# Optimization experiments

Measured on AMD Instinct MI355X. Metric: run time of the kernel, lower is better.

## Reference

```python
import jax, jax.numpy as jnp
import numpy as np

D_MODEL = 1024
M = 64            # oscillators; state dim N = 2*M
N = 2 * M
N_H = 2           # Householder reflections per step
DT = 0.1
OMEGA_MAX = 100.0
BATCH, SEQ = 8, 2048


def setup_inputs() -> dict:
    key = jax.random.key(0)
    ks = jax.random.split(key, 8)
    u = jax.random.normal(ks[0], (BATCH, SEQ, D_MODEL), jnp.float32)
    # learned parameters (scaled like the module's small-gain init)
    W_A = jax.random.normal(ks[1], (M, D_MODEL), jnp.float32) * 0.01
    b_A = jnp.zeros((M,), jnp.float32)
    W_k = jax.random.normal(ks[2], (N_H, N, D_MODEL), jnp.float32) * 0.02
    b_k = jnp.zeros((N_H, N), jnp.float32)
    W_beta = jax.random.normal(ks[3], (N_H, D_MODEL), jnp.float32) * 0.02
    b_beta = jnp.zeros((N_H,), jnp.float32)
    B_w = jax.random.normal(ks[4], (N, D_MODEL), jnp.float32) * 0.02
    B_b = jnp.zeros((N,), jnp.float32)
    C = jax.random.normal(ks[5], (D_MODEL, N), jnp.float32) * 0.01
    D = jax.random.normal(ks[6], (D_MODEL,), jnp.float32) * 0.01
    return dict(u=u, W_A=W_A, b_A=b_A, W_k=W_k, b_k=b_k,
                W_beta=W_beta, b_beta=b_beta, B_w=B_w, B_b=B_b, C=C, D=D)


def reference(u, W_A, b_A, W_k, b_k, W_beta, b_beta, B_w, B_b, C, D):
    batch = u.shape[0]
    # --- precompute all input-dependent per-step quantities as big GEMMs ---
    A = jax.nn.relu(jnp.einsum('btd,md->btm', u, W_A) + b_A)
    A = jnp.minimum(A, OMEGA_MAX)                       # clamp(max=omega_max)
    S = 1.0 / (1.0 + (DT * DT) * A)                     # (B,T,M)
    K = jnp.einsum('btd,jnd->btjn', u, W_k) + b_k       # (B,T,n_h,N)
    K = K / jnp.maximum(jnp.linalg.norm(K, axis=-1, keepdims=True), 1e-12)
    beta = 2.0 * jax.nn.sigmoid(jnp.einsum('btd,jd->btj', u, W_beta) + b_beta)
    Bt = jnp.einsum('btd,nd->btn', u, B_w) + B_b        # (B,T,N)

    # time-major for scan
    xs = (jnp.moveaxis(A, 1, 0), jnp.moveaxis(S, 1, 0), jnp.moveaxis(K, 1, 0),
          jnp.moveaxis(beta, 1, 0), jnp.moveaxis(Bt, 1, 0))
    h0 = jnp.zeros((batch, N), u.dtype)

    def step(h, x):
        A_t, S_t, K_t, beta_t, B_t = x
        # oscillatory rotation-contraction R_t @ h (m 2x2 blocks)
        z, y = h[:, :M], h[:, M:]
        z_new = S_t * z - DT * A_t * S_t * y
        y_new = DT * S_t * z + S_t * y
        h = jnp.concatenate([z_new, y_new], axis=-1)
        # sequential Householder product H_t @ h (fixed small n_h loop)
        for j in range(N_H):
            k = K_t[:, j]                                # (B,N), unit norm
            dot = jnp.sum(k * h, axis=-1, keepdims=True)
            h = h - beta_t[:, j:j + 1] * k * dot
        h = h + B_t
        return h, h

    _, hs = jax.lax.scan(step, h0, xs)                  # (T,B,N)
    hs = jnp.moveaxis(hs, 0, 1)                         # (B,T,N)
    return jnp.einsum('btn,dn->btd', hs, C) + u * D
```

## Files before the change

kernel.cpp:

```cpp
#include <hip/hip_runtime.h>
#include <cmath>


#define NTOK 16384
#define TT 2048
#define BB 8
#define DM 1024
#define FS 520
#define CH 64
#define LCH 32
#define NCH 512
#define NW 448
#define NWP 512

typedef short bf16x8 __attribute__((ext_vector_type(8)));
typedef float f32x4 __attribute__((ext_vector_type(4)));

#define GLOAD_LDS16(g, l)                                          \
  __builtin_amdgcn_global_load_lds(                                \
      (const __attribute__((address_space(1))) void*)(g),          \
      (__attribute__((address_space(3))) void*)(l), 16, 0, 0)

#define RAW_BAR() do {                                             \
    asm volatile("s_waitcnt lgkmcnt(0)" ::: "memory");             \
    __builtin_amdgcn_sched_barrier(0);                             \
    __builtin_amdgcn_s_barrier();                                  \
    __builtin_amdgcn_sched_barrier(0);                             \
  } while (0)

#define WAIT_VM(N) do {                                            \
    __builtin_amdgcn_sched_barrier(0);                             \
    asm volatile("s_waitcnt vmcnt(" #N ")" ::: "memory");          \
    __builtin_amdgcn_sched_barrier(0);                             \
  } while (0)

__global__ __launch_bounds__(256) void packW(
    const float* __restrict__ W_A, const float* __restrict__ b_A,
    const float* __restrict__ W_k, const float* __restrict__ b_k,
    const float* __restrict__ b_beta,
    const float* __restrict__ B_w, const float* __restrict__ B_b,
    float* __restrict__ Wp, float* __restrict__ bias) {
  int r = blockIdx.x;
  int tid = threadIdx.x;
  const float* src;
  float bv;
  if (r < 64)       { src = W_A + (size_t)r * DM;         bv = b_A[r]; }
  else if (r < 320) { src = W_k + (size_t)(r - 64) * DM;  bv = b_k[r - 64]; }
  else              { src = B_w + (size_t)(r - 320) * DM; bv = B_b[r - 320]; }
  ((float4*)(Wp + (size_t)r * DM))[tid] = ((const float4*)src)[tid];
  if (tid == 0) bias[r] = bv;
  if (r == 0 && tid < 2) bias[448 + tid] = b_beta[tid];
}

__device__ inline unsigned short bf16_rne(float x) {
  unsigned b = __float_as_uint(x);
  b += 0x7FFFu + ((b >> 16) & 1u);
  return (unsigned short)(b >> 16);
}

__device__ inline void split_bf16(float x, unsigned short& h, unsigned short& l) {
  unsigned b = __float_as_uint(x);
  h = (unsigned short)(b >> 16);
  float rem = x - __uint_as_float(b & 0xFFFF0000u);
  l = bf16_rne(rem);
}

__global__ __launch_bounds__(256) void convertU(
    const float* __restrict__ u, unsigned short* __restrict__ uh,
    unsigned short* __restrict__ ul) {
  int gid = blockIdx.x * 256 + threadIdx.x;
  int m = gid >> 8;
  int g = gid & 255;
  float4 v = *(const float4*)(u + (size_t)m * DM + g * 4);
  int kt = g >> 3, gg = g & 7;
  int p = gg & 3, h = gg >> 2;
  int mr = m & 127, mb = m >> 7;
  int pp = p ^ ((mr >> 2) & 3);
  size_t dst = ((size_t)(mb * 32 + kt)) * 4096 + mr * 32 + ((pp << 1) | h) * 4;
  ushort4 hi, lo;
  split_bf16(v.x, hi.x, lo.x);
  split_bf16(v.y, hi.y, lo.y);
  split_bf16(v.z, hi.z, lo.z);
  split_bf16(v.w, hi.w, lo.w);
  *(ushort4*)(uh + dst) = hi;
  *(ushort4*)(ul + dst) = lo;
}

__global__ __launch_bounds__(256) void convertW(
    const float* __restrict__ Wp, unsigned short* __restrict__ Wb) {
  int gid = blockIdx.x * 256 + threadIdx.x;
  int n = gid >> 8, g = gid & 255;
  int kt = g >> 3, gg = g & 7;
  int p = gg & 3, h = gg >> 2;
  int nr = n & 127, nb = n >> 7;
  int pp = p ^ ((nr >> 2) & 3);
  size_t dst = ((size_t)(nb * 32 + kt)) * 4096 + nr * 32 + ((pp << 1) | h) * 4;
  ushort4 hv = make_ushort4(0, 0, 0, 0);
  if (n < NW) {
    float4 v = *(const float4*)(Wp + (size_t)n * DM + g * 4);
    hv.x = bf16_rne(v.x); hv.y = bf16_rne(v.y);
    hv.z = bf16_rne(v.z); hv.w = bf16_rne(v.w);
  }
  *(ushort4*)(Wb + dst) = hv;
}

__global__ __launch_bounds__(256) void convertC(
    const float* __restrict__ Cm, unsigned short* __restrict__ Chp,
    unsigned short* __restrict__ Clp) {
  int gid = blockIdx.x * 256 + threadIdx.x;
  int d = gid >> 5;
  int g = gid & 31;
  float4 v = *(const float4*)(Cm + (size_t)d * 128 + g * 4);
  int kt = g >> 3, gg = g & 7;
  int p = gg & 3, h = gg >> 2;
  int nr = d & 127, nb = d >> 7;
  int pp = p ^ ((nr >> 2) & 3);
  size_t dst = ((size_t)(nb * 4 + kt)) * 4096 + nr * 32 + ((pp << 1) | h) * 4;
  ushort4 hi, lo;
  split_bf16(v.x, hi.x, lo.x);
  split_bf16(v.y, hi.y, lo.y);
  split_bf16(v.z, hi.z, lo.z);
  split_bf16(v.w, hi.w, lo.w);
  *(ushort4*)(Chp + dst) = hi;
  *(ushort4*)(Clp + dst) = lo;
}

__global__ __launch_bounds__(256) void gemmA_mfma(
    const unsigned short* __restrict__ uh, const unsigned short* __restrict__ ul,
    const unsigned short* __restrict__ Wb, float* __restrict__ Feat) {
  __shared__ __align__(16) unsigned short As[8192];
  __shared__ __align__(16) unsigned short Bs[8192];
  const int tid = threadIdx.x;
  const int wv = tid >> 6, ln = tid & 63;
  const int lr = ln & 15, G = ln >> 4;
  const int wm = wv >> 1, wn = wv & 1;
  const int x = G ^ (lr >> 2);
  f32x4 acc[4][4];
#pragma unroll
  for (int i = 0; i < 4; ++i)
#pragma unroll
    for (int j = 0; j < 4; ++j) acc[i][j] = (f32x4){0.f, 0.f, 0.f, 0.f};

  const size_t aBase = (size_t)blockIdx.x * 32 * 4096;
  const size_t bBase = (size_t)blockIdx.y * 32 * 4096;
  const int so = wv * 512 + ln * 8;
  const int ld = wv * 512;

  auto stage = [&](int step, int buf) {
    const unsigned short* pa = (step < 32) ? uh : ul;
    const int kt = step & 31;
    const unsigned short* ga = pa + aBase + (size_t)kt * 4096;
    const unsigned short* gb = Wb + bBase + (size_t)kt * 4096;
    unsigned short* A = As + buf * 4096;
    unsigned short* B = Bs + buf * 4096;
    GLOAD_LDS16(ga + so,        A + ld);
    GLOAD_LDS16(ga + 2048 + so, A + 2048 + ld);
    GLOAD_LDS16(gb + so,        B + ld);
    GLOAD_LDS16(gb + 2048 + so, B + 2048 + ld);
  };

  stage(0, 0);
  __syncthreads();
  for (int s = 0; s < 64; ++s) {
    const int cur = s & 1;
    if (s + 1 < 64) stage(s + 1, cur ^ 1);
    bf16x8 af[4], bfr[4];
    const char* Ab = (const char*)(As + cur * 4096) + ((wm * 64 + lr) << 6) + (x << 4);
    const char* Bb = (const char*)(Bs + cur * 4096) + ((wn * 64 + lr) << 6) + (x << 4);
#pragma unroll
    for (int i = 0; i < 4; ++i) {
      af[i]  = *(const bf16x8*)(Ab + i * 1024);
      bfr[i] = *(const bf16x8*)(Bb + i * 1024);
    }
#pragma unroll
    for (int i = 0; i < 4; ++i)
#pragma unroll
      for (int j = 0; j < 4; ++j)
        acc[i][j] = __builtin_amdgcn_mfma_f32_16x16x32_bf16(
            af[i], bfr[j], acc[i][j], 0, 0, 0);
    __syncthreads();
  }
  const int row0 = (blockIdx.x << 7) + wm * 64 + (G << 2);
  const int col0 = (blockIdx.y << 7) + wn * 64 + lr;
  float* fb = Feat + (size_t)row0 * FS + col0;
#pragma unroll
  for (int i = 0; i < 4; ++i)
#pragma unroll
    for (int j = 0; j < 4; ++j) {
      float* d = fb + (size_t)(i * 16) * FS + j * 16;
#pragma unroll
      for (int r = 0; r < 4; ++r) d[(size_t)r * FS] = acc[i][j][r];
    }
}

__global__ __launch_bounds__(256) void gemmC_mfma(
    const unsigned short* __restrict__ hsh, const unsigned short* __restrict__ hsl,
    const unsigned short* __restrict__ Chp, const unsigned short* __restrict__ Clp,
    const float* __restrict__ u, const float* __restrict__ Dv,
    float* __restrict__ out) {
  __shared__ __align__(16) unsigned short As[8192];
  __shared__ __align__(16) unsigned short Bs[8192];
  const int tid = threadIdx.x;
  const int wv = tid >> 6, ln = tid & 63;
  const int lr = ln & 15, G = ln >> 4;
  const int wm = wv >> 1, wn = wv & 1;
  const int x = G ^ (lr >> 2);
  f32x4 acc[4][4];
#pragma unroll
  for (int i = 0; i < 4; ++i)
#pragma unroll
    for (int j = 0; j < 4; ++j) acc[i][j] = (f32x4){0.f, 0.f, 0.f, 0.f};

  const size_t aBase = (size_t)blockIdx.x * 4 * 4096;
  const size_t bBase = (size_t)blockIdx.y * 4 * 4096;
  const int so = wv * 512 + ln * 8;
  const int ld = wv * 512;

  auto stage = [&](int step, int buf) {
    const int pass = step >> 2, kt = step & 3;
    const unsigned short* pa = (pass == 1) ? hsl : hsh;
    const unsigned short* pb = (pass == 2) ? Clp : Chp;
    const unsigned short* ga = pa + aBase + (size_t)kt * 4096;
    const unsigned short* gb = pb + bBase + (size_t)kt * 4096;
    unsigned short* A = As + buf * 4096;
    unsigned short* B = Bs + buf * 4096;
    GLOAD_LDS16(ga + so,        A + ld);
    GLOAD_LDS16(ga + 2048 + so, A + 2048 + ld);
    GLOAD_LDS16(gb + so,        B + ld);
    GLOAD_LDS16(gb + 2048 + so, B + 2048 + ld);
  };

  stage(0, 0);
  __syncthreads();
  for (int s = 0; s < 12; ++s) {
    const int cur = s & 1;
    if (s + 1 < 12) stage(s + 1, cur ^ 1);
    bf16x8 af[4], bfr[4];
    const char* Ab = (const char*)(As + cur * 4096) + ((wm * 64 + lr) << 6) + (x << 4);
    const char* Bb = (const char*)(Bs + cur * 4096) + ((wn * 64 + lr) << 6) + (x << 4);
#pragma unroll
    for (int i = 0; i < 4; ++i) {
      af[i]  = *(const bf16x8*)(Ab + i * 1024);
      bfr[i] = *(const bf16x8*)(Bb + i * 1024);
    }
#pragma unroll
    for (int i = 0; i < 4; ++i)
#pragma unroll
      for (int j = 0; j < 4; ++j)
        acc[i][j] = __builtin_amdgcn_mfma_f32_16x16x32_bf16(
            af[i], bfr[j], acc[i][j], 0, 0, 0);
    __syncthreads();
  }
  const int row0 = (blockIdx.x << 7) + wm * 64 + (G << 2);
  const int col0 = (blockIdx.y << 7) + wn * 64 + lr;
#pragma unroll
  for (int j = 0; j < 4; ++j) {
    float dv = Dv[col0 + j * 16];
#pragma unroll
    for (int i = 0; i < 4; ++i) {
#pragma unroll
      for (int r = 0; r < 4; ++r) {
        size_t off = (size_t)(row0 + i * 16 + r) * DM + col0 + j * 16;
        out[off] = fmaf(u[off], dv, acc[i][j][r]);
      }
    }
  }
}

__device__ inline float wave_sum(float v) {
#pragma unroll
  for (int off = 32; off > 0; off >>= 1) v += __shfl_xor(v, off, 64);
  return v;
}

__global__ __launch_bounds__(64) void postA(float* __restrict__ Feat,
                                            const float* __restrict__ bias,
                                            const float* __restrict__ u,
                                            const float* __restrict__ Wb) {
  const int t = blockIdx.x, lane = threadIdx.x;
  float* f = Feat + (size_t)t * FS;
  float s0 = 0.f, s1 = 0.f;
#pragma unroll
  for (int j = 0; j < 4; ++j) {
    float4 uv = *(const float4*)(u + (size_t)t * DM + j * 256 + lane * 4);
    float4 w0 = *(const float4*)(Wb + j * 256 + lane * 4);
    float4 w1 = *(const float4*)(Wb + DM + j * 256 + lane * 4);
    s0 = fmaf(uv.x, w0.x, s0); s0 = fmaf(uv.y, w0.y, s0);
    s0 = fmaf(uv.z, w0.z, s0); s0 = fmaf(uv.w, w0.w, s0);
    s1 = fmaf(uv.x, w1.x, s1); s1 = fmaf(uv.y, w1.y, s1);
    s1 = fmaf(uv.z, w1.z, s1); s1 = fmaf(uv.w, w1.w, s1);
  }
  s0 = wave_sum(s0); s1 = wave_sum(s1);
  float a = f[lane] + bias[lane];
  a = fminf(fmaxf(a, 0.f), 100.f);
  float S = 1.f / (1.f + 0.01f * a);
  f[lane] = S;
  f[448 + lane] = 0.1f * a * S;
  float k10 = f[64 + lane] + bias[64 + lane];
  float k11 = f[128 + lane] + bias[128 + lane];
  float n1 = wave_sum(k10 * k10 + k11 * k11);
  float inv1 = 1.f / fmaxf(sqrtf(n1), 1e-12f);
  k10 *= inv1; k11 *= inv1;
  f[64 + lane] = k10; f[128 + lane] = k11;
  float k20 = f[192 + lane] + bias[192 + lane];
  float k21 = f[256 + lane] + bias[256 + lane];
  float n2 = wave_sum(k20 * k20 + k21 * k21);
  float inv2 = 1.f / fmaxf(sqrtf(n2), 1e-12f);
  k20 *= inv2; k21 *= inv2;
  f[192 + lane] = k20; f[256 + lane] = k21;
  float c12 = wave_sum(k10 * k20 + k11 * k21);
  if (lane == 0) {
    f[512] = 2.f / (1.f + expf(-(s0 + bias[448])));
    f[513] = 2.f / (1.f + expf(-(s1 + bias[449])));
    f[514] = c12;
  }
  f[320 + lane] += bias[320 + lane];
  f[384 + lane] += bias[384 + lane];
}

__global__ __launch_bounds__(512, 2) void scanB1(
    const float* __restrict__ Feat, float* __restrict__ Mc) {
  const int cid = blockIdx.x;
  const int t0 = (cid >> 6) * TT + (cid & 63) * LCH;
  const int tid = threadIdx.x;
  const int col = tid >> 2, q = tid & 3;
  const int i0 = q * 16;
  __shared__ float fb[2][4 * FS];
  float mz[16], my[16];
#pragma unroll
  for (int j = 0; j < 16; ++j) {
    mz[j] = (i0 + j == col) ? 1.f : 0.f;
    my[j] = (64 + i0 + j == col) ? 1.f : 0.f;
  }
  {
    const float4* src = (const float4*)(Feat + (size_t)t0 * FS);
    for (int v = tid; v < FS; v += 512) ((float4*)fb[0])[v] = src[v];
  }
  __syncthreads();
  for (int g = 0; g < LCH / 4; ++g) {
    const int cur = g & 1;
    float4 pf0, pf1;
    const bool has2 = tid < (FS - 512);
    if (g < LCH / 4 - 1) {
      const float4* src = (const float4*)(Feat + (size_t)(t0 + (g + 1) * 4) * FS);
      pf0 = src[tid];
      if (has2) pf1 = src[tid + 512];
    }
#pragma unroll
    for (int s = 0; s < 4; ++s) {
      const float* f = fb[cur] + s * FS;
      float sj[16], cj[16], k1z[16], k1y[16], k2z[16], k2y[16];
#pragma unroll
      for (int v = 0; v < 4; ++v) {
        *(float4*)&sj[4 * v]  = *(const float4*)(f + i0 + 4 * v);
        *(float4*)&cj[4 * v]  = *(const float4*)(f + 448 + i0 + 4 * v);
        *(float4*)&k1z[4 * v] = *(const float4*)(f + 64 + i0 + 4 * v);
        *(float4*)&k1y[4 * v] = *(const float4*)(f + 128 + i0 + 4 * v);
        *(float4*)&k2z[4 * v] = *(const float4*)(f + 192 + i0 + 4 * v);
        *(float4*)&k2y[4 * v] = *(const float4*)(f + 256 + i0 + 4 * v);
      }
      float4 sc = *(const float4*)(f + 512);
      float p = 0.f, r2 = 0.f;
#pragma unroll
      for (int j = 0; j < 16; ++j) {
        float s0 = sj[j], c1 = cj[j];
        float z = mz[j], y = my[j];
        float sz = s0 * z;
        z = fmaf(-c1, y, sz);
        y = fmaf(s0, y, 0.1f * sz);
        mz[j] = z; my[j] = y;
        p  = fmaf(k1z[j], z, p);  p  = fmaf(k1y[j], y, p);
        r2 = fmaf(k2z[j], z, r2); r2 = fmaf(k2y[j], y, r2);
      }
      p  += __shfl_xor(p, 1, 64);  p  += __shfl_xor(p, 2, 64);
      r2 += __shfl_xor(r2, 1, 64); r2 += __shfl_xor(r2, 2, 64);
      float e1 = sc.x * p;
      float e2 = sc.y * fmaf(-sc.z, e1, r2);
#pragma unroll
      for (int j = 0; j < 16; ++j) {
        float z = fmaf(-e1, k1z[j], mz[j]);
        mz[j] = fmaf(-e2, k2z[j], z);
        float y = fmaf(-e1, k1y[j], my[j]);
        my[j] = fmaf(-e2, k2y[j], y);
      }
    }
    if (g < LCH / 4 - 1) {
      ((float4*)fb[1 - cur])[tid] = pf0;
      if (has2) ((float4*)fb[1 - cur])[tid + 512] = pf1;
    }
    __syncthreads();
  }
  float* dst = Mc + ((size_t)cid * 128 + col) * 128;
#pragma unroll
  for (int v = 0; v < 4; ++v)
    *(float4*)(dst + i0 + 4 * v) = *(float4*)&mz[4 * v];
#pragma unroll
  for (int v = 0; v < 4; ++v)
    *(float4*)(dst + 64 + i0 + 4 * v) = *(float4*)&my[4 * v];
}

__global__ __launch_bounds__(64) void scanB0(
    const float* __restrict__ Feat, float* __restrict__ dc) {
  const int cid = blockIdx.x;
  const int lane = threadIdx.x;
  float z = 0.f, y = 0.f;
  const int t0 = (cid >> 6) * TT + (cid & 63) * LCH;
  for (int t = t0; t < t0 + LCH; ++t) {
    const float* __restrict__ f = Feat + (size_t)t * FS;
    float s = f[lane], c1 = f[448 + lane];
    float k1z = f[64 + lane], k1y = f[128 + lane];
    float k2z = f[192 + lane], k2y = f[256 + lane];
    float bz = f[320 + lane], by = f[384 + lane];
    float b1 = f[512], b2 = f[513], c12 = f[514];
    float sz = s * z;
    float zn = fmaf(-c1, y, sz);
    float yn = fmaf(s, y, 0.1f * sz);
    float p = fmaf(k1y, yn, k1z * zn);
    float qq = fmaf(k2y, yn, k2z * zn);
#pragma unroll
    for (int off = 32; off > 0; off >>= 1) {
      p += __shfl_xor(p, off, 64);
      qq += __shfl_xor(qq, off, 64);
    }
    float e1 = b1 * p;
    float d2 = fmaf(-c12, e1, qq);
    float e2 = b2 * d2;
    z = fmaf(-e1, k1z, zn); z = fmaf(-e2, k2z, z); z += bz;
    y = fmaf(-e1, k1y, yn); y = fmaf(-e2, k2y, y); y += by;
  }
  dc[(size_t)cid * 128 + lane] = z;
  dc[(size_t)cid * 128 + 64 + lane] = y;
}

__global__ __launch_bounds__(1024, 1) void scanB2(
    const float* __restrict__ Mc, const float* __restrict__ dc,
    float* __restrict__ hstart) {
  const int b = blockIdx.x;
  const int tid = threadIdx.x;
  const int i = tid & 127, jh = tid >> 7;
  const int wv = tid >> 6;
  __shared__ __align__(16) float Ms[2][16384];
  __shared__ float h[128];
  __shared__ float red[8][128];
  if (tid < 128) h[tid] = 0.f;

  auto stage = [&](int cn, int buf) {
    const float* g = Mc + (size_t)(b * CH + cn) * 16384;
#pragma unroll
    for (int q = 0; q < 4; ++q) {
      const float* gp = g + q * 4096 + wv * 256 + (tid & 63) * 4;
      float* lp = Ms[buf] + q * 4096 + wv * 256;
      GLOAD_LDS16(gp, lp);
    }
  };

  stage(0, 0);
  float d0 = dc[(size_t)(b * CH) * 128 + i];
  __syncthreads();

  int cur = 0;
  for (int c = 0; c < CH; ++c) {
    const int cn = (c + 1) & (CH - 1);
    stage(cn, cur ^ 1);
    float d1 = dc[(size_t)(b * CH + cn) * 128 + i];
    WAIT_VM(5);
    RAW_BAR();
    if (tid < 128) hstart[(size_t)(b * CH + c) * 128 + tid] = h[tid];
    float acc = 0.f;
#pragma unroll
    for (int j = 0; j < 16; ++j)
      acc = fmaf(Ms[cur][(jh * 16 + j) * 128 + i], h[jh * 16 + j], acc);
    red[jh][i] = acc;
    RAW_BAR();
    if (tid < 128) {
      float sum = d0;
#pragma unroll
      for (int k = 0; k < 8; ++k) sum += red[k][tid];
      h[tid] = sum;
    }
    d0 = d1;
    cur ^= 1;
  }
}

__global__ __launch_bounds__(64) void scanB3(
    const float* __restrict__ Feat, const float* __restrict__ hstart,
    unsigned short* __restrict__ hsh, unsigned short* __restrict__ hsl) {
  const int cid = blockIdx.x;
  const int lane = threadIdx.x;
  float z = hstart[(size_t)cid * 128 + lane];
  float y = hstart[(size_t)cid * 128 + 64 + lane];
  const int t0 = (cid >> 6) * TT + (cid & 63) * LCH;
  const int ktz = lane >> 5, kkz = lane & 31;
  const int kty = (64 + lane) >> 5;
  const int pz = (kkz >> 2) & 3, hz = kkz >> 4;
  const int lowz = kkz & 3;
  for (int t = t0; t < t0 + LCH; ++t) {
    const float* __restrict__ f = Feat + (size_t)t * FS;
    float s = f[lane], c1 = f[448 + lane];
    float k1z = f[64 + lane], k1y = f[128 + lane];
    float k2z = f[192 + lane], k2y = f[256 + lane];
    float bz = f[320 + lane], by = f[384 + lane];
    float b1 = f[512], b2 = f[513], c12 = f[514];
    float sz = s * z;
    float zn = fmaf(-c1, y, sz);
    float yn = fmaf(s, y, 0.1f * sz);
    float p = fmaf(k1y, yn, k1z * zn);
    float qq = fmaf(k2y, yn, k2z * zn);
#pragma unroll
    for (int off = 32; off > 0; off >>= 1) {
      p += __shfl_xor(p, off, 64);
      qq += __shfl_xor(qq, off, 64);
    }
    float e1 = b1 * p;
    float d2 = fmaf(-c12, e1, qq);
    float e2 = b2 * d2;
    zn = fmaf(-e1, k1z, zn); zn = fmaf(-e2, k2z, zn); zn += bz;
    yn = fmaf(-e1, k1y, yn); yn = fmaf(-e2, k2y, yn); yn += by;
    {
      const int mb = t >> 7, mr = t & 127;
      const int xr = (mr >> 2) & 3;
      size_t idxz = ((size_t)(mb * 4 + ktz)) * 4096 + mr * 32 +
                    ((((pz ^ xr) << 1) | hz)) * 4 + lowz;
      size_t idxy = ((size_t)(mb * 4 + kty)) * 4096 + mr * 32 +
                    ((((pz ^ xr) << 1) | hz)) * 4 + lowz;
      unsigned short hi, lo;
      split_bf16(zn, hi, lo);
      hsh[idxz] = hi; hsl[idxz] = lo;
      split_bf16(yn, hi, lo);
      hsh[idxy] = hi; hsl[idxy] = lo;
    }
    z = zn; y = yn;
  }
}

extern "C" void kernel_launch(void* const* d_in, const int* in_sizes, int n_in,
                              void* d_out, int out_size, void* d_ws, size_t ws_size,
                              hipStream_t stream) {
  const float* u      = (const float*)d_in[0];
  const float* W_A    = (const float*)d_in[1];
  const float* b_A    = (const float*)d_in[2];
  const float* W_k    = (const float*)d_in[3];
  const float* b_k    = (const float*)d_in[4];
  const float* W_beta = (const float*)d_in[5];
  const float* b_beta = (const float*)d_in[6];
  const float* B_w    = (const float*)d_in[7];
  const float* B_b    = (const float*)d_in[8];
  const float* Cm     = (const float*)d_in[9];
  const float* Dv     = (const float*)d_in[10];
  float* out = (float*)d_out;
  char* ws = (char*)d_ws;
  float* Wp     = (float*)(ws);
  unsigned short* Wb = (unsigned short*)(ws + 1835008);
  float* bias   = (float*)(ws + 4194304);
  float* Feat   = (float*)(ws + 4198400);
  unsigned short* uh = (unsigned short*)(ws + 38277120);
  float* Mc     = (float*)(ws + 38277120);
  unsigned short* ul = (unsigned short*)(ws + 71831552);
  unsigned short* hsh = (unsigned short*)(ws + 71831552);
  unsigned short* hsl = (unsigned short*)(ws + 76025856);
  unsigned short* Chp = (unsigned short*)(ws + 80220160);
  unsigned short* Clp = (unsigned short*)(ws + 80482304);
  float* dcv    = (float*)(ws + 80744448);
  float* hstart = (float*)(ws + 81006592);

  packW<<<dim3(448), dim3(256), 0, stream>>>(W_A, b_A, W_k, b_k, b_beta,
                                             B_w, B_b, Wp, bias);
  convertW<<<dim3(512), dim3(256), 0, stream>>>(Wp, Wb);
  convertU<<<dim3(16384), dim3(256), 0, stream>>>(u, uh, ul);
  gemmA_mfma<<<dim3(128, 4), dim3(256), 0, stream>>>(uh, ul, Wb, Feat);
  convertC<<<dim3(128), dim3(256), 0, stream>>>(Cm, Chp, Clp);
  postA<<<dim3(16384), dim3(64), 0, stream>>>(Feat, bias, u, W_beta);
  scanB1<<<dim3(NCH), dim3(512), 0, stream>>>(Feat, Mc);
  scanB0<<<dim3(NCH), dim3(64), 0, stream>>>(Feat, dcv);
  scanB2<<<dim3(8), dim3(1024), 0, stream>>>(Mc, dcv, hstart);
  scanB3<<<dim3(NCH), dim3(64), 0, stream>>>(Feat, hstart, hsh, hsl);
  gemmC_mfma<<<dim3(128, 8), dim3(256), 0, stream>>>(hsh, hsl, Chp, Clp,
                                                     u, Dv, out);
}
```

Measured before the change: 423.9 us.

## Split chunk-carry scan across four blocks per batch with global flag sync

The sequential chunk-carry propagation was one 1024-thread block per batch, streaming each 128x128 chunk matrix through LDS. It is now four 256-thread blocks per batch, each owning 32 output rows, which hold their matrix slice in registers and exchange the full state through global memory using per-chunk atomic counters with acquire/release spinning. The aim is to spread the serial chain across more CUs and cut per-step LDS staging and reduction. The cost is a cross-block global round-trip and spin-wait every chunk. It also relies on all 32 blocks being co-resident, and the spin loop has a timeout guard.

Result: slower. 500.0 us (+18.0%).

```diff
diff --git a/kernel.cpp b/kernel.cpp
--- a/kernel.cpp
+++ b/kernel.cpp
@@ -20,19 +20,6 @@
   __builtin_amdgcn_global_load_lds(                                \
       (const __attribute__((address_space(1))) void*)(g),          \
       (__attribute__((address_space(3))) void*)(l), 16, 0, 0)
-
-#define RAW_BAR() do {                                             \
-    asm volatile("s_waitcnt lgkmcnt(0)" ::: "memory");             \
-    __builtin_amdgcn_sched_barrier(0);                             \
-    __builtin_amdgcn_s_barrier();                                  \
-    __builtin_amdgcn_sched_barrier(0);                             \
-  } while (0)
-
-#define WAIT_VM(N) do {                                            \
-    __builtin_amdgcn_sched_barrier(0);                             \
-    asm volatile("s_waitcnt vmcnt(" #N ")" ::: "memory");          \
-    __builtin_amdgcn_sched_barrier(0);                             \
-  } while (0)
 
 __global__ __launch_bounds__(256) void packW(
     const float* __restrict__ W_A, const float* __restrict__ b_A,
@@ -400,9 +387,13 @@
 }
 
 __global__ __launch_bounds__(64) void scanB0(
-    const float* __restrict__ Feat, float* __restrict__ dc) {
+    const float* __restrict__ Feat, float* __restrict__ dc,
+    int* __restrict__ flags) {
   const int cid = blockIdx.x;
   const int lane = threadIdx.x;
+  if (cid == 0) {
+    for (int i = lane; i < 512; i += 64) flags[i] = 0;
+  }
   float z = 0.f, y = 0.f;
   const int t0 = (cid >> 6) * TT + (cid & 63) * LCH;
   for (int t = t0; t < t0 + LCH; ++t) {
@@ -432,54 +423,61 @@
   dc[(size_t)cid * 128 + 64 + lane] = y;
 }
 
-__global__ __launch_bounds__(1024, 1) void scanB2(
+__global__ __launch_bounds__(256) void scanB2x(
     const float* __restrict__ Mc, const float* __restrict__ dc,
-    float* __restrict__ hstart) {
-  const int b = blockIdx.x;
+    float* __restrict__ hstart, int* __restrict__ flags) {
+  const int bid = blockIdx.x;
+  const int b = bid >> 2, g = bid & 3;
   const int tid = threadIdx.x;
-  const int i = tid & 127, jh = tid >> 7;
-  const int wv = tid >> 6;
-  __shared__ __align__(16) float Ms[2][16384];
-  __shared__ float h[128];
-  __shared__ float red[8][128];
-  if (tid < 128) h[tid] = 0.f;
-
-  auto stage = [&](int cn, int buf) {
-    const float* g = Mc + (size_t)(b * CH + cn) * 16384;
-#pragma unroll
-    for (int q = 0; q < 4; ++q) {
-      const float* gp = g + q * 4096 + wv * 256 + (tid & 63) * 4;
-      float* lp = Ms[buf] + q * 4096 + wv * 256;
-      GLOAD_LDS16(gp, lp);
-    }
-  };
-
-  stage(0, 0);
-  float d0 = dc[(size_t)(b * CH) * 128 + i];
+  const int s = tid >> 5, r = tid & 31;
+  const int R = g * 32 + r;
+  __shared__ float dl[CH][32];
+  __shared__ float red[8][32];
+  __shared__ float hcur[128];
+  for (int idx = tid; idx < CH * 32; idx += 256) {
+    int c = idx >> 5, rr = idx & 31;
+    dl[c][rr] = dc[(size_t)(b * CH + c) * 128 + g * 32 + rr];
+  }
+  if (tid < 32) hstart[(size_t)(b * CH) * 128 + g * 32 + tid] = 0.f;
+  if (tid < 128) hcur[tid] = 0.f;
   __syncthreads();
 
-  int cur = 0;
   for (int c = 0; c < CH; ++c) {
-    const int cn = (c + 1) & (CH - 1);
-    stage(cn, cur ^ 1);
-    float d1 = dc[(size_t)(b * CH + cn) * 128 + i];
-    WAIT_VM(5);
-    RAW_BAR();
-    if (tid < 128) hstart[(size_t)(b * CH + c) * 128 + tid] = h[tid];
+    const float* Mp = Mc + ((size_t)(b * CH + c) * 128 + s * 16) * 128 + R;
+    float m[16];
+#pragma unroll
+    for (int j = 0; j < 16; ++j) m[j] = Mp[(size_t)j * 128];
+    if (c > 0) {
+      if (tid == 0) {
+        int guard = 0;
+        while (__hip_atomic_load(&flags[b * 64 + c], __ATOMIC_ACQUIRE,
+                                 __HIP_MEMORY_SCOPE_AGENT) < 4) {
+          __builtin_amdgcn_s_sleep(1);
+          if (++guard > (1 << 26)) break;
+        }
+      }
+      __syncthreads();
+      if (tid < 128) hcur[tid] = hstart[(size_t)(b * CH + c) * 128 + tid];
+      __syncthreads();
+    }
     float acc = 0.f;
 #pragma unroll
-    for (int j = 0; j < 16; ++j)
-      acc = fmaf(Ms[cur][(jh * 16 + j) * 128 + i], h[jh * 16 + j], acc);
-    red[jh][i] = acc;
-    RAW_BAR();
-    if (tid < 128) {
-      float sum = d0;
-#pragma unroll
-      for (int k = 0; k < 8; ++k) sum += red[k][tid];
-      h[tid] = sum;
-    }
-    d0 = d1;
-    cur ^= 1;
+    for (int j = 0; j < 16; ++j) acc = fmaf(m[j], hcur[s * 16 + j], acc);
+    red[s][r] = acc;
+    __syncthreads();
+    if (c + 1 < CH) {
+      if (tid < 32) {
+        float sum = dl[c][tid];
+#pragma unroll
+        for (int k = 0; k < 8; ++k) sum += red[k][tid];
+        hstart[(size_t)(b * CH + c + 1) * 128 + g * 32 + tid] = sum;
+        __threadfence();
+      }
+      __syncthreads();
+      if (tid == 0)
+        __hip_atomic_fetch_add(&flags[b * 64 + c + 1], 1, __ATOMIC_RELEASE,
+                               __HIP_MEMORY_SCOPE_AGENT);
+    }
   }
 }
 
@@ -563,6 +561,7 @@
   unsigned short* Clp = (unsigned short*)(ws + 80482304);
   float* dcv    = (float*)(ws + 80744448);
   float* hstart = (float*)(ws + 81006592);
+  int* flags    = (int*)(ws + 81268736);
 
   packW<<<dim3(448), dim3(256), 0, stream>>>(W_A, b_A, W_k, b_k, b_beta,
                                              B_w, B_b, Wp, bias);
@@ -572,8 +571,8 @@
   convertC<<<dim3(128), dim3(256), 0, stream>>>(Cm, Chp, Clp);
   postA<<<dim3(16384), dim3(64), 0, stream>>>(Feat, bias, u, W_beta);
   scanB1<<<dim3(NCH), dim3(512), 0, stream>>>(Feat, Mc);
-  scanB0<<<dim3(NCH), dim3(64), 0, stream>>>(Feat, dcv);
-  scanB2<<<dim3(8), dim3(1024), 0, stream>>>(Mc, dcv, hstart);
+  scanB0<<<dim3(NCH), dim3(64), 0, stream>>>(Feat, dcv, flags);
+  scanB2x<<<dim3(32), dim3(256), 0, stream>>>(Mc, dcv, hstart, flags);
   scanB3<<<dim3(NCH), dim3(64), 0, stream>>>(Feat, hstart, hsh, hsl);
   gemmC_mfma<<<dim3(128, 8), dim3(256), 0, stream>>>(hsh, hsl, Chp, Clp,
                                                      u, Dv, out);
```

## Fuse weight packing into convertW and register-prefetch Mc in scanB2

Applied to the files above, without the earlier changes.

Removes the packW kernel by having convertW read W_A/W_k/B_w directly and write the bias vector from one block, saving a launch and an intermediate fp32 copy. In scanB2, the double-buffered LDS staging of the 64KB chunk transition matrix via global_load_lds is replaced by per-thread register prefetch of 16 matrix entries for the next chunk. This trades LDS occupancy and async copies for register loads and adds an extra barrier per chunk.

New measurement: 401.6 us. 1.06x faster.

```diff
diff --git a/kernel.cpp b/kernel.cpp
--- a/kernel.cpp
+++ b/kernel.cpp
@@ -27,30 +27,6 @@
     __builtin_amdgcn_s_barrier();                                  \
     __builtin_amdgcn_sched_barrier(0);                             \
   } while (0)
-
-#define WAIT_VM(N) do {                                            \
-    __builtin_amdgcn_sched_barrier(0);                             \
-    asm volatile("s_waitcnt vmcnt(" #N ")" ::: "memory");          \
-    __builtin_amdgcn_sched_barrier(0);                             \
-  } while (0)
-
-__global__ __launch_bounds__(256) void packW(
-    const float* __restrict__ W_A, const float* __restrict__ b_A,
-    const float* __restrict__ W_k, const float* __restrict__ b_k,
-    const float* __restrict__ b_beta,
-    const float* __restrict__ B_w, const float* __restrict__ B_b,
-    float* __restrict__ Wp, float* __restrict__ bias) {
-  int r = blockIdx.x;
-  int tid = threadIdx.x;
-  const float* src;
-  float bv;
-  if (r < 64)       { src = W_A + (size_t)r * DM;         bv = b_A[r]; }
-  else if (r < 320) { src = W_k + (size_t)(r - 64) * DM;  bv = b_k[r - 64]; }
-  else              { src = B_w + (size_t)(r - 320) * DM; bv = B_b[r - 320]; }
-  ((float4*)(Wp + (size_t)r * DM))[tid] = ((const float4*)src)[tid];
-  if (tid == 0) bias[r] = bv;
-  if (r == 0 && tid < 2) bias[448 + tid] = b_beta[tid];
-}
 
 __device__ inline unsigned short bf16_rne(float x) {
   unsigned b = __float_as_uint(x);
@@ -87,9 +63,13 @@
 }
 
 __global__ __launch_bounds__(256) void convertW(
-    const float* __restrict__ Wp, unsigned short* __restrict__ Wb) {
-  int gid = blockIdx.x * 256 + threadIdx.x;
-  int n = gid >> 8, g = gid & 255;
+    const float* __restrict__ W_A, const float* __restrict__ W_k,
+    const float* __restrict__ B_w, const float* __restrict__ b_A,
+    const float* __restrict__ b_k, const float* __restrict__ B_b,
+    const float* __restrict__ b_beta, unsigned short* __restrict__ Wb,
+    float* __restrict__ bias) {
+  int n = blockIdx.x;
+  int g = threadIdx.x;
   int kt = g >> 3, gg = g & 7;
   int p = gg & 3, h = gg >> 2;
   int nr = n & 127, nb = n >> 7;
@@ -97,11 +77,25 @@
   size_t dst = ((size_t)(nb * 32 + kt)) * 4096 + nr * 32 + ((pp << 1) | h) * 4;
   ushort4 hv = make_ushort4(0, 0, 0, 0);
   if (n < NW) {
-    float4 v = *(const float4*)(Wp + (size_t)n * DM + g * 4);
+    const float* src;
+    if (n < 64)       src = W_A + (size_t)n * DM;
+    else if (n < 320) src = W_k + (size_t)(n - 64) * DM;
+    else              src = B_w + (size_t)(n - 320) * DM;
+    float4 v = *(const float4*)(src + g * 4);
     hv.x = bf16_rne(v.x); hv.y = bf16_rne(v.y);
     hv.z = bf16_rne(v.z); hv.w = bf16_rne(v.w);
   }
   *(ushort4*)(Wb + dst) = hv;
+  if (n == 448) {
+    for (int i = threadIdx.x; i < 450; i += 256) {
+      float bv;
+      if (i < 64)       bv = b_A[i];
+      else if (i < 320) bv = b_k[i - 64];
+      else if (i < 448) bv = B_b[i - 320];
+      else              bv = b_beta[i - 448];
+      bias[i] = bv;
+    }
+  }
 }
 
 __global__ __launch_bounds__(256) void convertC(
@@ -438,38 +432,28 @@
   const int b = blockIdx.x;
   const int tid = threadIdx.x;
   const int i = tid & 127, jh = tid >> 7;
-  const int wv = tid >> 6;
-  __shared__ __align__(16) float Ms[2][16384];
   __shared__ float h[128];
   __shared__ float red[8][128];
   if (tid < 128) h[tid] = 0.f;
-
-  auto stage = [&](int cn, int buf) {
-    const float* g = Mc + (size_t)(b * CH + cn) * 16384;
-#pragma unroll
-    for (int q = 0; q < 4; ++q) {
-      const float* gp = g + q * 4096 + wv * 256 + (tid & 63) * 4;
-      float* lp = Ms[buf] + q * 4096 + wv * 256;
-      GLOAD_LDS16(gp, lp);
-    }
-  };
-
-  stage(0, 0);
-  float d0 = dc[(size_t)(b * CH) * 128 + i];
   __syncthreads();
-
-  int cur = 0;
+  float ma[16], mb[16];
+  float d0, d1;
+  {
+    const float* M0 = Mc + (size_t)(b * CH) * 16384;
+#pragma unroll
+    for (int j = 0; j < 16; ++j) ma[j] = M0[(size_t)(jh * 16 + j) * 128 + i];
+    d0 = dc[(size_t)(b * CH) * 128 + i];
+  }
   for (int c = 0; c < CH; ++c) {
-    const int cn = (c + 1) & (CH - 1);
-    stage(cn, cur ^ 1);
-    float d1 = dc[(size_t)(b * CH + cn) * 128 + i];
-    WAIT_VM(5);
-    RAW_BAR();
+    const int cn = (c + 1 < CH) ? c + 1 : c;
+    const float* Mn = Mc + (size_t)(b * CH + cn) * 16384;
+#pragma unroll
+    for (int j = 0; j < 16; ++j) mb[j] = Mn[(size_t)(jh * 16 + j) * 128 + i];
+    d1 = dc[(size_t)(b * CH + cn) * 128 + i];
     if (tid < 128) hstart[(size_t)(b * CH + c) * 128 + tid] = h[tid];
     float acc = 0.f;
 #pragma unroll
-    for (int j = 0; j < 16; ++j)
-      acc = fmaf(Ms[cur][(jh * 16 + j) * 128 + i], h[jh * 16 + j], acc);
+    for (int j = 0; j < 16; ++j) acc = fmaf(ma[j], h[jh * 16 + j], acc);
     red[jh][i] = acc;
     RAW_BAR();
     if (tid < 128) {
@@ -478,8 +462,10 @@
       for (int k = 0; k < 8; ++k) sum += red[k][tid];
       h[tid] = sum;
     }
+    RAW_BAR();
+#pragma unroll
+    for (int j = 0; j < 16; ++j) ma[j] = mb[j];
     d0 = d1;
-    cur ^= 1;
   }
 }
 
@@ -550,7 +536,6 @@
   const float* Dv     = (const float*)d_in[10];
   float* out = (float*)d_out;
   char* ws = (char*)d_ws;
-  float* Wp     = (float*)(ws);
   unsigned short* Wb = (unsigned short*)(ws + 1835008);
   float* bias   = (float*)(ws + 4194304);
   float* Feat   = (float*)(ws + 4198400);
@@ -564,9 +549,8 @@
   float* dcv    = (float*)(ws + 80744448);
   float* hstart = (float*)(ws + 81006592);
 
-  packW<<<dim3(448), dim3(256), 0, stream>>>(W_A, b_A, W_k, b_k, b_beta,
-                                             B_w, B_b, Wp, bias);
-  convertW<<<dim3(512), dim3(256), 0, stream>>>(Wp, Wb);
+  convertW<<<dim3(512), dim3(256), 0, stream>>>(W_A, W_k, B_w, b_A, b_k,
+                                                B_b, b_beta, Wb, bias);
   convertU<<<dim3(16384), dim3(256), 0, stream>>>(u, uh, ul);
   gemmA_mfma<<<dim3(128, 4), dim3(256), 0, stream>>>(uh, ul, Wb, Feat);
   convertC<<<dim3(128), dim3(256), 0, stream>>>(Cm, Chp, Clp);
```
